# Kernel tuning notes

Measured on AMD Instinct MI355X. Metric: run time of the kernel, lower is better.

Reference implementation:

```python
import jax, jax.numpy as jnp
import numpy as np

ALPHA = 0.2  # leaky relu slope
NEG = -9e15

N, NFEAT, NHID, NHEADS = 4096, 1024, 64, 8
EMB = NHID * NHEADS  # 512


def setup_inputs() -> dict:
    key = jax.random.key(0)
    ks = jax.random.split(key, 16)
    x = jax.random.normal(ks[0], (N, NFEAT), dtype=jnp.float32)
    adj = (jax.random.uniform(ks[1], (N, N)) < 0.01).astype(jnp.float32)
    adj = jnp.maximum(adj, jnp.eye(N, dtype=jnp.float32))
    s = 0.05
    W = jax.random.normal(ks[2], (NHEADS, NFEAT, NHID), dtype=jnp.float32) * s
    a1 = jax.random.normal(ks[3], (NHEADS, NHID), dtype=jnp.float32) * s
    a2 = jax.random.normal(ks[4], (NHEADS, NHID), dtype=jnp.float32) * s
    # decoder: 512 -> 256 -> 256 -> 512 -> 1024 (PyTorch Linear convention: y = x @ W.T + b)
    W1 = jax.random.normal(ks[5], (EMB // 2, EMB), dtype=jnp.float32) * s
    b1 = jnp.zeros((EMB // 2,), dtype=jnp.float32)
    W2 = jax.random.normal(ks[6], (NFEAT // 4, EMB // 2), dtype=jnp.float32) * s
    b2 = jnp.zeros((NFEAT // 4,), dtype=jnp.float32)
    W3 = jax.random.normal(ks[7], (NFEAT // 2, NFEAT // 4), dtype=jnp.float32) * s
    b3 = jnp.zeros((NFEAT // 2,), dtype=jnp.float32)
    W4 = jax.random.normal(ks[8], (NFEAT, NFEAT // 2), dtype=jnp.float32) * s
    b4 = jnp.zeros((NFEAT,), dtype=jnp.float32)
    return {"x": x, "adj": adj, "W": W, "a1": a1, "a2": a2,
            "W1": W1, "b1": b1, "W2": W2, "b2": b2,
            "W3": W3, "b3": b3, "W4": W4, "b4": b4}


def reference(x, adj, W, a1, a2, W1, b1, W2, b2, W3, b3, W4, b4):
    # --- encoder: multi-head GAT (dropout=0) ---
    Wh = jnp.einsum('nf,hfd->hnd', x, W)              # [H, N, nhid]
    e_src = jnp.einsum('hnd,hd->hn', Wh, a1)          # [H, N]
    e_dst = jnp.einsum('hnd,hd->hn', Wh, a2)          # [H, N]
    e = jax.nn.leaky_relu(e_src[:, :, None] + e_dst[:, None, :], ALPHA)  # [H, N, N]
    e = jnp.where(adj[None] > 0, e, NEG)
    att = jax.nn.softmax(e, axis=-1)
    h = jnp.einsum('hnm,hmd->hnd', att, Wh)           # [H, N, nhid]
    h = jax.nn.elu(h)                                 # concat=True -> elu per layer
    enc = jnp.transpose(h, (1, 0, 2)).reshape(x.shape[0], -1)  # [N, H*nhid]
    # --- decoder: 4-layer MLP ---
    out = jax.nn.relu(enc @ W1.T + b1)
    out = jax.nn.relu(out @ W2.T + b2)
    out = jax.nn.relu(out @ W3.T + b3)
    out = out @ W4.T + b4
    return out
```

## Files before the change

### kernel.cpp

```cpp
#include <hip/hip_runtime.h>
#include <hip/hip_bf16.h>
#include <math.h>

#define NNODES 4096
#define NFEAT_ 1024
#define NHID_  64
#define NHEADS_ 8
#define EMB_   512
#define MAXD   256
constexpr float ALPHA_ = 0.2f;

typedef __attribute__((ext_vector_type(8))) short bf16x8;
typedef __attribute__((ext_vector_type(4))) float f32x4;
typedef unsigned int u32;
typedef unsigned short u16;

__device__ inline u16 f2b(float f) {
    __hip_bfloat16 b = __float2bfloat16(f);
    return *(u16*)&b;
}
__device__ inline float b2f(u16 u) {
    return __uint_as_float(((u32)u) << 16);
}

__device__ inline void cp16(const void* g, void* l) {
    __builtin_amdgcn_global_load_lds(
        (const __attribute__((address_space(1))) u32*)g,
        (__attribute__((address_space(3))) u32*)l, 16, 0, 0);
}

template<int BM, int BN, int OUTM, int ACT, bool SCORES>
__global__ __launch_bounds__(256) void gemm_bt(
    const u16* __restrict__ A, const u16* __restrict__ B,
    const float* __restrict__ bias, void* __restrict__ Cv,
    const float* __restrict__ a1, const float* __restrict__ a2,
    float* __restrict__ es, float* __restrict__ ed,
    int M, int N, int K)
{
    constexpr int BK  = 32;
    constexpr int WM  = BM / 2;
    constexpr int MI  = WM / 16;
    constexpr int WN  = BN / 2;
    constexpr int NJ  = WN / 16;
    constexpr int ACH = BM / 16;
    constexpr int BCH = BN / 16;
    static_assert(!SCORES || BN == 64, "SCORES assumes one head per block");

    __shared__ __align__(16) u16 As[2][BM * BK];
    __shared__ __align__(16) u16 Bs[2][BN * BK];
    __shared__ float s1Lds[SCORES ? 2 : 1][SCORES ? BM : 1];
    __shared__ float s2Lds[SCORES ? 2 : 1][SCORES ? BM : 1];

    const int tid  = threadIdx.x;
    const int wid  = tid >> 6, lane = tid & 63;
    const int wr   = wid >> 1, wc = wid & 1;
    const int m0   = blockIdx.y * BM, n0 = blockIdx.x * BN;
    const int frow = lane & 15, fk = (lane >> 4) * 8;
    const int lr   = lane >> 2, lc = (lane & 3) * 8;

    auto stage = [&](int buf, int k0) {
        const u16* gA = A + (long)m0 * K + k0;
        {
            int c = wid;
            cp16(gA + (long)(c * 16 + lr) * K + lc, &As[buf][c * 512]);
            if (ACH == 8) {
                c = wid + 4;
                cp16(gA + (long)(c * 16 + lr) * K + lc, &As[buf][c * 512]);
            }
        }
        const u16* gB = B + (long)n0 * K + k0;
        if (BCH >= 4) {
            int c = wid;
            cp16(gB + (long)(c * 16 + lr) * K + lc, &Bs[buf][c * 512]);
            if (BCH == 8) {
                c = wid + 4;
                cp16(gB + (long)(c * 16 + lr) * K + lc, &Bs[buf][c * 512]);
            }
        } else if (wid < BCH) {
            cp16(gB + (long)(wid * 16 + lr) * K + lc, &Bs[buf][wid * 512]);
        }
    };

    f32x4 acc[MI][NJ] = {};

    stage(0, 0);
    __syncthreads();
    int cur = 0;
    for (int k0 = 0; k0 < K; k0 += BK) {
        if (k0 + BK < K) stage(cur ^ 1, k0 + BK);

        bf16x8 af[MI], bfr[NJ];
        #pragma unroll
        for (int i = 0; i < MI; ++i)
            af[i] = *(const bf16x8*)&As[cur][(wr * WM + i * 16 + frow) * BK + fk];
        #pragma unroll
        for (int j = 0; j < NJ; ++j)
            bfr[j] = *(const bf16x8*)&Bs[cur][(wc * WN + j * 16 + frow) * BK + fk];
        #pragma unroll
        for (int i = 0; i < MI; ++i)
            #pragma unroll
            for (int j = 0; j < NJ; ++j)
                acc[i][j] = __builtin_amdgcn_mfma_f32_16x16x32_bf16(
                    af[i], bfr[j], acc[i][j], 0, 0, 0);

        __syncthreads();
        cur ^= 1;
    }

    const int crow0 = m0 + wr * WM + (lane >> 4) * 4;
    const int ccol0 = n0 + wc * WN + (lane & 15);
    #pragma unroll
    for (int i = 0; i < MI; ++i)
        #pragma unroll
        for (int j = 0; j < NJ; ++j)
            #pragma unroll
            for (int r = 0; r < 4; ++r) {
                const int row = crow0 + i * 16 + r;
                const int col = ccol0 + j * 16;
                float v = acc[i][j][r];
                if (bias) v += bias[col];
                if (ACT == 1) v = v > 0.f ? v : 0.f;
                if (OUTM == 1) ((u16*)Cv)[(long)row * N + col] = f2b(v);
                else           ((float*)Cv)[(long)row * N + col] = v;
            }

    if constexpr (SCORES) {
        const int h = n0 >> 6;
        const float a1v0 = a1[h * 64 + wc * WN + frow];
        const float a1v1 = a1[h * 64 + wc * WN + 16 + frow];
        const float a2v0 = a2[h * 64 + wc * WN + frow];
        const float a2v1 = a2[h * 64 + wc * WN + 16 + frow];
        #pragma unroll
        for (int i = 0; i < MI; ++i)
            #pragma unroll
            for (int r = 0; r < 4; ++r) {
                float s1 = acc[i][0][r] * a1v0 + acc[i][1][r] * a1v1;
                float s2 = acc[i][0][r] * a2v0 + acc[i][1][r] * a2v1;
                #pragma unroll
                for (int off = 8; off; off >>= 1) {
                    s1 += __shfl_xor(s1, off);
                    s2 += __shfl_xor(s2, off);
                }
                if (frow == 0) {
                    const int row = wr * WM + i * 16 + (lane >> 4) * 4 + r;
                    s1Lds[wc][row] = s1;
                    s2Lds[wc][row] = s2;
                }
            }
        __syncthreads();
        if (tid < BM) {
            es[h * NNODES + m0 + tid] = s1Lds[0][tid] + s1Lds[1][tid];
            ed[h * NNODES + m0 + tid] = s2Lds[0][tid] + s2Lds[1][tid];
        }
    }
}

__global__ __launch_bounds__(256) void prep_nbr(
    const float* __restrict__ x,   const float* __restrict__ adj,
    const float* __restrict__ W,
    const float* __restrict__ W1,  const float* __restrict__ W2,
    const float* __restrict__ W3,  const float* __restrict__ W4,
    u16* __restrict__ xb,  u16* __restrict__ WcT,
    u16* __restrict__ W1b, u16* __restrict__ W2b,
    u16* __restrict__ W3b, u16* __restrict__ W4b,
    int* __restrict__ cnt, int* __restrict__ nbr)
{
    const int b = blockIdx.x, tid = threadIdx.x;

    if (b < NNODES) {
        __shared__ int lcnt;
        if (tid == 0) lcnt = 0;
        __syncthreads();
        const float4* arow = (const float4*)(adj + (long)b * NNODES);
        for (int m4 = tid; m4 < NNODES / 4; m4 += 256) {
            const float4 v = arow[m4];
            if (v.x != 0.f) { const int p = atomicAdd(&lcnt, 1); if (p < MAXD) nbr[b * MAXD + p] = m4 * 4; }
            if (v.y != 0.f) { const int p = atomicAdd(&lcnt, 1); if (p < MAXD) nbr[b * MAXD + p] = m4 * 4 + 1; }
            if (v.z != 0.f) { const int p = atomicAdd(&lcnt, 1); if (p < MAXD) nbr[b * MAXD + p] = m4 * 4 + 2; }
            if (v.w != 0.f) { const int p = atomicAdd(&lcnt, 1); if (p < MAXD) nbr[b * MAXD + p] = m4 * 4 + 3; }
        }
        __syncthreads();
        if (tid == 0) cnt[b] = lcnt < MAXD ? lcnt : MAXD;
    } else if (b < NNODES + 128) {
        __shared__ float tile[64][65];
        const int tb = b - NNODES;
        const int h = tb >> 4, k0 = (tb & 15) * 64;
        #pragma unroll
        for (int p = 0; p < 4; ++p) {
            const int kr = p * 16 + (tid >> 4), d = (tid & 15) * 4;
            const float4 v = *(const float4*)&W[((long)h * NFEAT_ + k0 + kr) * NHID_ + d];
            tile[kr][d] = v.x; tile[kr][d + 1] = v.y;
            tile[kr][d + 2] = v.z; tile[kr][d + 3] = v.w;
        }
        __syncthreads();
        #pragma unroll
        for (int p = 0; p < 4; ++p) {
            const int d = p * 16 + (tid >> 4), k = (tid & 15) * 4;
            ushort4 o;
            o.x = f2b(tile[k][d]);     o.y = f2b(tile[k + 1][d]);
            o.z = f2b(tile[k + 2][d]); o.w = f2b(tile[k + 3][d]);
            *(ushort4*)&WcT[((long)h * 64 + d) * NFEAT_ + k0 + k] = o;
        }
    } else {
        const int np = 256 * 256;
        const int t = (b - NNODES - 128) * 256 + tid;
        for (int i = t; i < (NNODES * NFEAT_) / 4; i += np) {
            const float4 v = ((const float4*)x)[i];
            ushort4 o; o.x = f2b(v.x); o.y = f2b(v.y); o.z = f2b(v.z); o.w = f2b(v.w);
            ((ushort4*)xb)[i] = o;
        }
        for (int i = t; i < (256 * 512) / 4; i += np) {
            const float4 v = ((const float4*)W1)[i];
            ushort4 o; o.x = f2b(v.x); o.y = f2b(v.y); o.z = f2b(v.z); o.w = f2b(v.w);
            ((ushort4*)W1b)[i] = o;
        }
        for (int i = t; i < (256 * 256) / 4; i += np) {
            const float4 v = ((const float4*)W2)[i];
            ushort4 o; o.x = f2b(v.x); o.y = f2b(v.y); o.z = f2b(v.z); o.w = f2b(v.w);
            ((ushort4*)W2b)[i] = o;
        }
        for (int i = t; i < (512 * 256) / 4; i += np) {
            const float4 v = ((const float4*)W3)[i];
            ushort4 o; o.x = f2b(v.x); o.y = f2b(v.y); o.z = f2b(v.z); o.w = f2b(v.w);
            ((ushort4*)W3b)[i] = o;
        }
        for (int i = t; i < (1024 * 512) / 4; i += np) {
            const float4 v = ((const float4*)W4)[i];
            ushort4 o; o.x = f2b(v.x); o.y = f2b(v.y); o.z = f2b(v.z); o.w = f2b(v.w);
            ((ushort4*)W4b)[i] = o;
        }
    }
}

__global__ __launch_bounds__(256) void attn_agg(
    const u16* __restrict__ Whb, const float* __restrict__ esrc,
    const float* __restrict__ edst, const int* __restrict__ cnt,
    const int* __restrict__ nbr, u16* __restrict__ enc)
{
    __shared__ __align__(16) float pLds[4][MAXD];
    __shared__ __align__(16) int   mLds[4][MAXD];
    const int w = threadIdx.x >> 6, lane = threadIdx.x & 63;
    const int pair = blockIdx.x * 4 + w;
    const int h = pair >> 12, n = pair & 4095;

    const int deg  = min(cnt[n], MAXD);
    const int degp = (deg + 15) & ~15;
    const int* lst = nbr + n * MAXD;
    const float es = esrc[h * NNODES + n];

    float mymax = -3.4e38f;
    for (int j = lane; j < deg; j += 64) {
        const int m = lst[j];
        float ev = es + edst[h * NNODES + m];
        ev = ev > 0.f ? ev : ALPHA_ * ev;
        pLds[w][j] = ev;
        mLds[w][j] = m;
        mymax = fmaxf(mymax, ev);
    }
    for (int j = deg + lane; j < degp; j += 64) {
        pLds[w][j] = 0.f;
        mLds[w][j] = 0;
    }
    #pragma unroll
    for (int off = 32; off; off >>= 1) mymax = fmaxf(mymax, __shfl_xor(mymax, off));

    float mysum = 0.f;
    for (int j = lane; j < deg; j += 64) {
        const float p = __expf(pLds[w][j] - mymax);
        pLds[w][j] = p;
        mysum += p;
    }
    #pragma unroll
    for (int off = 32; off; off >>= 1) mysum += __shfl_xor(mysum, off);

    __syncthreads();

    float acc = 0.f;
    const u16* base = Whb + (long)h * NHID_ + lane;
    for (int j0 = 0; j0 < degp; j0 += 16) {
        const int4   ma = *(const int4*)&mLds[w][j0];
        const int4   mb = *(const int4*)&mLds[w][j0 + 4];
        const int4   mc = *(const int4*)&mLds[w][j0 + 8];
        const int4   md = *(const int4*)&mLds[w][j0 + 12];
        const float4 pa = *(const float4*)&pLds[w][j0];
        const float4 pb = *(const float4*)&pLds[w][j0 + 4];
        const float4 pc = *(const float4*)&pLds[w][j0 + 8];
        const float4 pd = *(const float4*)&pLds[w][j0 + 12];
        const float v0  = b2f(base[(long)ma.x << 9]);
        const float v1  = b2f(base[(long)ma.y << 9]);
        const float v2  = b2f(base[(long)ma.z << 9]);
        const float v3  = b2f(base[(long)ma.w << 9]);
        const float v4  = b2f(base[(long)mb.x << 9]);
        const float v5  = b2f(base[(long)mb.y << 9]);
        const float v6  = b2f(base[(long)mb.z << 9]);
        const float v7  = b2f(base[(long)mb.w << 9]);
        const float v8  = b2f(base[(long)mc.x << 9]);
        const float v9  = b2f(base[(long)mc.y << 9]);
        const float v10 = b2f(base[(long)mc.z << 9]);
        const float v11 = b2f(base[(long)mc.w << 9]);
        const float v12 = b2f(base[(long)md.x << 9]);
        const float v13 = b2f(base[(long)md.y << 9]);
        const float v14 = b2f(base[(long)md.z << 9]);
        const float v15 = b2f(base[(long)md.w << 9]);
        acc = fmaf(pa.x, v0,  acc); acc = fmaf(pa.y, v1,  acc);
        acc = fmaf(pa.z, v2,  acc); acc = fmaf(pa.w, v3,  acc);
        acc = fmaf(pb.x, v4,  acc); acc = fmaf(pb.y, v5,  acc);
        acc = fmaf(pb.z, v6,  acc); acc = fmaf(pb.w, v7,  acc);
        acc = fmaf(pc.x, v8,  acc); acc = fmaf(pc.y, v9,  acc);
        acc = fmaf(pc.z, v10, acc); acc = fmaf(pc.w, v11, acc);
        acc = fmaf(pd.x, v12, acc); acc = fmaf(pd.y, v13, acc);
        acc = fmaf(pd.z, v14, acc); acc = fmaf(pd.w, v15, acc);
    }

    float hv = acc / mysum;
    hv = hv > 0.f ? hv : expm1f(hv);
    enc[(long)n * EMB_ + h * NHID_ + lane] = f2b(hv);
}

extern "C" void kernel_launch(void* const* d_in, const int* in_sizes, int n_in,
                              void* d_out, int out_size, void* d_ws, size_t ws_size,
                              hipStream_t stream)
{
    const float* x   = (const float*)d_in[0];
    const float* adj = (const float*)d_in[1];
    const float* W   = (const float*)d_in[2];
    const float* a1  = (const float*)d_in[3];
    const float* a2  = (const float*)d_in[4];
    const float* W1  = (const float*)d_in[5];
    const float* b1  = (const float*)d_in[6];
    const float* W2  = (const float*)d_in[7];
    const float* b2  = (const float*)d_in[8];
    const float* W3  = (const float*)d_in[9];
    const float* b3  = (const float*)d_in[10];
    const float* W4  = (const float*)d_in[11];
    const float* b4  = (const float*)d_in[12];
    float* out = (float*)d_out;

    float* es  = (float*)d_ws;
    float* ed  = es + 32768;
    u16* Whb = (u16*)(ed + 32768);
    u16* enc = Whb + 2097152;
    u16* WcT = enc + 2097152;
    u16* W1b = WcT + 524288;
    u16* W2b = W1b + 131072;
    u16* W3b = W2b + 65536;
    u16* W4b = W3b + 131072;
    int* cnt = (int*)(W4b + 524288);
    int* nbr = cnt + 4096;
    u16* xb  = (u16*)(nbr + 1048576);
    u16* dd1 = xb;
    u16* dd2 = dd1 + 1048576;
    u16* dd3 = dd2 + 1048576;

    prep_nbr<<<dim3(NNODES + 128 + 256), 256, 0, stream>>>(
        x, adj, W, W1, W2, W3, W4, xb, WcT, W1b, W2b, W3b, W4b, cnt, nbr);

    gemm_bt<64, 64, 1, 0, true><<<dim3(8, 64), 256, 0, stream>>>(
        xb, WcT, nullptr, Whb, a1, a2, es, ed, NNODES, EMB_, NFEAT_);

    attn_agg<<<dim3(8192), 256, 0, stream>>>(Whb, es, ed, cnt, nbr, enc);

    gemm_bt<64, 32, 1, 1, false><<<dim3(8, 64), 256, 0, stream>>>(
        enc, W1b, b1, dd1, nullptr, nullptr, nullptr, nullptr, NNODES, 256, 512);
    gemm_bt<64, 32, 1, 1, false><<<dim3(8, 64), 256, 0, stream>>>(
        dd1, W2b, b2, dd2, nullptr, nullptr, nullptr, nullptr, NNODES, 256, 256);
    gemm_bt<64, 64, 1, 1, false><<<dim3(8, 64), 256, 0, stream>>>(
        dd2, W3b, b3, dd3, nullptr, nullptr, nullptr, nullptr, NNODES, 512, 256);
    gemm_bt<128, 128, 0, 0, false><<<dim3(8, 32), 256, 0, stream>>>(
        dd3, W4b, b4, out, nullptr, nullptr, nullptr, nullptr, NNODES, 1024, 512);
}
```

Baseline: 229.7 us.

## Process all heads per node in one attention block and enlarge GEMM M-tiles

The attention kernel now runs one 512-thread block per node, one wave per head. The neighbor list is loaded into LDS once and shared across the eight heads, and e_dst is stored node-major so each neighbor's eight head scores sit together. All GEMMs switch to a fixed 128-row M tile, halving the grid rows to cut per-block overhead and reuse B tiles more. Larger tiles lower block count and occupancy for the small decoder GEMMs, and the bigger attention block adds a barrier across waves whose nodes differ in degree.

```diff
diff --git a/kernel.cpp b/kernel.cpp
--- a/kernel.cpp
+++ b/kernel.cpp
@@ -29,20 +29,19 @@
         (__attribute__((address_space(3))) u32*)l, 16, 0, 0);
 }
 
-template<int BM, int BN, int OUTM, int ACT, bool SCORES>
+template<int BN, int OUTM, int ACT, bool SCORES>
 __global__ __launch_bounds__(256) void gemm_bt(
     const u16* __restrict__ A, const u16* __restrict__ B,
     const float* __restrict__ bias, void* __restrict__ Cv,
     const float* __restrict__ a1, const float* __restrict__ a2,
-    float* __restrict__ es, float* __restrict__ ed,
+    float* __restrict__ es, float* __restrict__ edT,
     int M, int N, int K)
 {
-    constexpr int BK  = 32;
+    constexpr int BM  = 128, BK = 32;
     constexpr int WM  = BM / 2;
     constexpr int MI  = WM / 16;
     constexpr int WN  = BN / 2;
     constexpr int NJ  = WN / 16;
-    constexpr int ACH = BM / 16;
     constexpr int BCH = BN / 16;
     static_assert(!SCORES || BN == 64, "SCORES assumes one head per block");
 
@@ -60,17 +59,13 @@
 
     auto stage = [&](int buf, int k0) {
         const u16* gA = A + (long)m0 * K + k0;
-        {
-            int c = wid;
-            cp16(gA + (long)(c * 16 + lr) * K + lc, &As[buf][c * 512]);
-            if (ACH == 8) {
-                c = wid + 4;
-                cp16(gA + (long)(c * 16 + lr) * K + lc, &As[buf][c * 512]);
-            }
-        }
+        int c = wid;
+        cp16(gA + (long)(c * 16 + lr) * K + lc, &As[buf][c * 512]);
+        c = wid + 4;
+        cp16(gA + (long)(c * 16 + lr) * K + lc, &As[buf][c * 512]);
         const u16* gB = B + (long)n0 * K + k0;
         if (BCH >= 4) {
-            int c = wid;
+            c = wid;
             cp16(gB + (long)(c * 16 + lr) * K + lc, &Bs[buf][c * 512]);
             if (BCH == 8) {
                 c = wid + 4;
@@ -150,7 +145,7 @@
         __syncthreads();
         if (tid < BM) {
             es[h * NNODES + m0 + tid] = s1Lds[0][tid] + s1Lds[1][tid];
-            ed[h * NNODES + m0 + tid] = s2Lds[0][tid] + s2Lds[1][tid];
+            edT[(m0 + tid) * NHEADS_ + h] = s2Lds[0][tid] + s2Lds[1][tid];
         }
     }
 }
@@ -232,42 +227,43 @@
     }
 }
 
-__global__ __launch_bounds__(256) void attn_agg(
+__global__ __launch_bounds__(512) void attn_agg(
     const u16* __restrict__ Whb, const float* __restrict__ esrc,
-    const float* __restrict__ edst, const int* __restrict__ cnt,
+    const float* __restrict__ edT, const int* __restrict__ cnt,
     const int* __restrict__ nbr, u16* __restrict__ enc)
 {
-    __shared__ __align__(16) float pLds[4][MAXD];
-    __shared__ __align__(16) int   mLds[4][MAXD];
-    const int w = threadIdx.x >> 6, lane = threadIdx.x & 63;
-    const int pair = blockIdx.x * 4 + w;
-    const int h = pair >> 12, n = pair & 4095;
+    __shared__ __align__(16) int   mLds[MAXD];
+    __shared__ __align__(16) float pLds[NHEADS_][MAXD];
+    const int h = threadIdx.x >> 6, lane = threadIdx.x & 63;
+    const int n = blockIdx.x;
 
     const int deg  = min(cnt[n], MAXD);
     const int degp = (deg + 15) & ~15;
-    const int* lst = nbr + n * MAXD;
+
+    if (h == 0) {
+        const int* lst = nbr + n * MAXD;
+        for (int j = lane; j < deg; j += 64) mLds[j] = lst[j];
+        for (int j = deg + lane; j < degp; j += 64) mLds[j] = 0;
+    }
+    __syncthreads();
+
     const float es = esrc[h * NNODES + n];
 
     float mymax = -3.4e38f;
     for (int j = lane; j < deg; j += 64) {
-        const int m = lst[j];
-        float ev = es + edst[h * NNODES + m];
+        float ev = es + edT[mLds[j] * NHEADS_ + h];
         ev = ev > 0.f ? ev : ALPHA_ * ev;
-        pLds[w][j] = ev;
-        mLds[w][j] = m;
+        pLds[h][j] = ev;
         mymax = fmaxf(mymax, ev);
     }
-    for (int j = deg + lane; j < degp; j += 64) {
-        pLds[w][j] = 0.f;
-        mLds[w][j] = 0;
-    }
+    for (int j = deg + lane; j < degp; j += 64) pLds[h][j] = 0.f;
     #pragma unroll
     for (int off = 32; off; off >>= 1) mymax = fmaxf(mymax, __shfl_xor(mymax, off));
 
     float mysum = 0.f;
     for (int j = lane; j < deg; j += 64) {
-        const float p = __expf(pLds[w][j] - mymax);
-        pLds[w][j] = p;
+        const float p = __expf(pLds[h][j] - mymax);
+        pLds[h][j] = p;
         mysum += p;
     }
     #pragma unroll
@@ -276,16 +272,16 @@
     __syncthreads();
 
     float acc = 0.f;
-    const u16* base = Whb + (long)h * NHID_ + lane;
+    const u16* base = Whb + h * NHID_ + lane;
     for (int j0 = 0; j0 < degp; j0 += 16) {
-        const int4   ma = *(const int4*)&mLds[w][j0];
-        const int4   mb = *(const int4*)&mLds[w][j0 + 4];
-        const int4   mc = *(const int4*)&mLds[w][j0 + 8];
-        const int4   md = *(const int4*)&mLds[w][j0 + 12];
-        const float4 pa = *(const float4*)&pLds[w][j0];
-        const float4 pb = *(const float4*)&pLds[w][j0 + 4];
-        const float4 pc = *(const float4*)&pLds[w][j0 + 8];
-        const float4 pd = *(const float4*)&pLds[w][j0 + 12];
+        const int4   ma = *(const int4*)&mLds[j0];
+        const int4   mb = *(const int4*)&mLds[j0 + 4];
+        const int4   mc = *(const int4*)&mLds[j0 + 8];
+        const int4   md = *(const int4*)&mLds[j0 + 12];
+        const float4 pa = *(const float4*)&pLds[h][j0];
+        const float4 pb = *(const float4*)&pLds[h][j0 + 4];
+        const float4 pc = *(const float4*)&pLds[h][j0 + 8];
+        const float4 pd = *(const float4*)&pLds[h][j0 + 12];
         const float v0  = b2f(base[(long)ma.x << 9]);
         const float v1  = b2f(base[(long)ma.y << 9]);
         const float v2  = b2f(base[(long)ma.z << 9]);
@@ -337,8 +333,8 @@
     float* out = (float*)d_out;
 
     float* es  = (float*)d_ws;
-    float* ed  = es + 32768;
-    u16* Whb = (u16*)(ed + 32768);
+    float* edT = es + 32768;
+    u16* Whb = (u16*)(edT + 32768);
     u16* enc = Whb + 2097152;
     u16* WcT = enc + 2097152;
     u16* W1b = WcT + 524288;
@@ -355,17 +351,17 @@
     prep_nbr<<<dim3(NNODES + 128 + 256), 256, 0, stream>>>(
         x, adj, W, W1, W2, W3, W4, xb, WcT, W1b, W2b, W3b, W4b, cnt, nbr);
 
-    gemm_bt<64, 64, 1, 0, true><<<dim3(8, 64), 256, 0, stream>>>(
-        xb, WcT, nullptr, Whb, a1, a2, es, ed, NNODES, EMB_, NFEAT_);
-
-    attn_agg<<<dim3(8192), 256, 0, stream>>>(Whb, es, ed, cnt, nbr, enc);
-
-    gemm_bt<64, 32, 1, 1, false><<<dim3(8, 64), 256, 0, stream>>>(
+    gemm_bt<64, 1, 0, true><<<dim3(8, 32), 256, 0, stream>>>(
+        xb, WcT, nullptr, Whb, a1, a2, es, edT, NNODES, EMB_, NFEAT_);
+
+    attn_agg<<<dim3(NNODES), 512, 0, stream>>>(Whb, es, edT, cnt, nbr, enc);
+
+    gemm_bt<32, 1, 1, false><<<dim3(8, 32), 256, 0, stream>>>(
         enc, W1b, b1, dd1, nullptr, nullptr, nullptr, nullptr, NNODES, 256, 512);
-    gemm_bt<64, 32, 1, 1, false><<<dim3(8, 64), 256, 0, stream>>>(
+    gemm_bt<32, 1, 1, false><<<dim3(8, 32), 256, 0, stream>>>(
         dd1, W2b, b2, dd2, nullptr, nullptr, nullptr, nullptr, NNODES, 256, 256);
-    gemm_bt<64, 64, 1, 1, false><<<dim3(8, 64), 256, 0, stream>>>(
+    gemm_bt<64, 1, 1, false><<<dim3(8, 32), 256, 0, stream>>>(
         dd2, W3b, b3, dd3, nullptr, nullptr, nullptr, nullptr, NNODES, 512, 256);
-    gemm_bt<128, 128, 0, 0, false><<<dim3(8, 32), 256, 0, stream>>>(
+    gemm_bt<128, 0, 0, false><<<dim3(8, 32), 256, 0, stream>>>(
         dd3, W4b, b4, out, nullptr, nullptr, nullptr, nullptr, NNODES, 1024, 512);
 }
```

Measured after the change: 243.0 us. 1.06x slower.
